# Optimization experiments

Hardware: AMD Instinct MI355X
Metric: run time of the kernel (lower is better)

The kernel has to match this reference:

```python
import jax, jax.numpy as jnp
import numpy as np

NTOKEN, NINP, NHID = 32000, 512, 1024
B, T = 64, 512


def setup_inputs() -> dict:
    key = jax.random.key(0)
    ks = jax.random.split(key, 12)
    inp = {}
    inp["input"] = jax.random.randint(ks[0], (B, T), 0, NTOKEN, dtype=jnp.int64)
    inp["hx"] = jnp.zeros((B, NHID), jnp.float32)
    inp["cx"] = jnp.zeros((B, NHID), jnp.float32)
    inp["seq_len"] = jax.random.randint(ks[1], (B,), 1, T + 1, dtype=jnp.int64)
    # parameters
    inp["emb_table"] = jax.random.uniform(ks[2], (NTOKEN, NINP), jnp.float32, -0.1, 0.1)
    s_ih = 1.0 / np.sqrt(NHID)
    inp["W_ih"] = jax.random.uniform(ks[3], (4 * NHID, NINP), jnp.float32, -s_ih, s_ih)
    inp["W_hh"] = jax.random.uniform(ks[4], (4 * NHID, NHID), jnp.float32, -s_ih, s_ih)
    inp["b_ih"] = jax.random.uniform(ks[5], (4 * NHID,), jnp.float32, -s_ih, s_ih)
    inp["b_hh"] = jax.random.uniform(ks[6], (4 * NHID,), jnp.float32, -s_ih, s_ih)
    h3 = NHID // 3
    s1 = 1.0 / np.sqrt(NHID)
    inp["fc1_W"] = jax.random.uniform(ks[7], (h3, NHID), jnp.float32, -s1, s1)
    inp["fc1_b"] = jax.random.uniform(ks[8], (h3,), jnp.float32, -s1, s1)
    s2 = 1.0 / np.sqrt(h3)
    inp["fc2_W"] = jax.random.uniform(ks[9], (2, h3), jnp.float32, -s2, s2)
    inp["fc2_b"] = jax.random.uniform(ks[10], (2,), jnp.float32, -s2, s2)
    return inp


def reference(input, hx, cx, seq_len, emb_table, W_ih, W_hh, b_ih, b_hh,
              fc1_W, fc1_b, fc2_W, fc2_b):
    # emb: [T, B, ninp] (input is [B, T], transposed as in torch)
    emb = emb_table[input.T]
    # precompute input projections for all timesteps: [T, B, 4H]
    x_proj = jnp.einsum('tbi,gi->tbg', emb, W_ih) + b_ih + b_hh

    def step(carry, xg):
        h, c = carry
        gates = xg + h @ W_hh.T  # [B, 4H]
        i, f, g, o = jnp.split(gates, 4, axis=-1)
        i = jax.nn.sigmoid(i)
        f = jax.nn.sigmoid(f)
        g = jnp.tanh(g)
        o = jax.nn.sigmoid(o)
        c = f * c + i * g
        h = o * jnp.tanh(c)
        return (h, c), h

    (hx, cx), outs = jax.lax.scan(step, (hx, cx), x_proj)  # outs: [T, B, H]

    # ragged mean pool over valid timesteps t < seq_len[b]
    t = outs.shape[0]
    mask = (jnp.arange(t)[:, None] < seq_len[None, :]).astype(outs.dtype)  # [T, B]
    feature = jnp.einsum('tbh,tb->bh', outs, mask) / seq_len[:, None].astype(outs.dtype)

    x = feature @ fc1_W.T + fc1_b
    x = x @ fc2_W.T + fc2_b
    logp = jax.nn.log_softmax(x, axis=-1)
    return logp, hx, cx
```

## Files before the change

### kernel.cpp

```cpp
#include <hip/hip_runtime.h>
#include <stdint.h>

#define NTOK  32000
#define NINP  512
#define NHID  1024
#define NBATCH 64
#define NTIME 512
#define NGATE 4096
#define H3    341

typedef __attribute__((ext_vector_type(8))) short  short8;
typedef __attribute__((ext_vector_type(4))) float  floatx4;
typedef unsigned long long ull;

#define HBUF_DW (NBATCH * NHID / 2)

__device__ __forceinline__ unsigned short f2bf(float f) {
  union { float f; unsigned u; } v; v.f = f;
  unsigned r = v.u + 0x7fffu + ((v.u >> 16) & 1u);
  return (unsigned short)(r >> 16);
}
__device__ __forceinline__ float bf2f(unsigned short h) {
  union { unsigned u; float f; } v; v.u = ((unsigned)h) << 16;
  return v.f;
}

__device__ __forceinline__ int pack2gate(int p) {
  int cb = p >> 7, r7 = p & 127;
  int w = r7 >> 5, r5 = r7 & 31;
  int uu = r5 >> 2, q = r5 & 3;
  int u = cb * 32 + w * 8 + uu;
  return q * NHID + u;
}


__global__ void k_pack_w(const float* __restrict__ src, unsigned short* __restrict__ dst, int K) {
  int p = blockIdx.x;
  int g = pack2gate(p);
  const float* s = src + (size_t)g * K;
  unsigned short* d = dst + (size_t)p * K;
  for (int k = threadIdx.x * 2; k < K; k += 512) {
    d[k] = f2bf(s[k]);
    d[k + 1] = f2bf(s[k + 1]);
  }
}

__global__ void k_bias(const float* __restrict__ bih, const float* __restrict__ bhh,
                       float* __restrict__ bp) {
  int p = blockIdx.x * 256 + threadIdx.x;
  if (p < NGATE) { int g = pack2gate(p); bp[p] = bih[g] + bhh[g]; }
}

__global__ void k_hbuf(const float* __restrict__ hx, unsigned short* __restrict__ hbuf) {
  int i = blockIdx.x * 256 + threadIdx.x;
  if (i < NBATCH * NHID) hbuf[i] = f2bf(hx[i]);
}

__global__ void k_gather(const int* __restrict__ input, const float* __restrict__ emb,
                         unsigned short* __restrict__ Ag, int t0, int Tc) {
  int total = Tc * 64 * (NINP / 8);
  for (int ci = blockIdx.x * 256 + threadIdx.x; ci < total; ci += gridDim.x * 256) {
    int row = ci >> 6;
    int k8 = (ci & 63) * 8;
    int b = row & 63;
    int tl = row >> 6;
    int tok = input[(size_t)b * NTIME + t0 + tl];
    const float* s = emb + (size_t)tok * NINP + k8;
    unsigned short* d = Ag + (size_t)row * NINP + k8;
#pragma unroll
    for (int j = 0; j < 8; ++j) d[j] = f2bf(s[j]);
  }
}


__global__ __launch_bounds__(256) void k_gemm(const unsigned short* __restrict__ Ag,
                                              const unsigned short* __restrict__ Wp,
                                              const float* __restrict__ biasP,
                                              unsigned short* __restrict__ xproj, int M) {
  __shared__ __attribute__((aligned(16))) unsigned short As[128 * 64];
  __shared__ __attribute__((aligned(16))) unsigned short Bs[128 * 64];
  const int tid = threadIdx.x;
  const int lane = tid & 63;
  const int w = tid >> 6;
  const int wr = w >> 1, wc = w & 1;
  const size_t rowbase = (size_t)blockIdx.x * 128;
  const int pbase = blockIdx.y * 128;

  floatx4 z = {0.f, 0.f, 0.f, 0.f};
  floatx4 acc[4][4];
#pragma unroll
  for (int i = 0; i < 4; ++i)
#pragma unroll
    for (int j = 0; j < 4; ++j) acc[i][j] = z;

  for (int kk = 0; kk < NINP; kk += 64) {
#pragma unroll
    for (int j = 0; j < 4; ++j) {
      int ci = j * 256 + tid;
      int r = ci >> 3;
      int kb = (ci & 7) * 16;
      int dst = r * 128 + (kb ^ ((r & 7) << 4));
      *(short8*)((char*)As + dst) =
          *(const short8*)((const char*)Ag + ((rowbase + r) * NINP + kk) * 2 + kb);
      *(short8*)((char*)Bs + dst) =
          *(const short8*)((const char*)Wp + ((size_t)(pbase + r) * NINP + kk) * 2 + kb);
    }
    __syncthreads();
#pragma unroll
    for (int k32 = 0; k32 < 2; ++k32) {
      short8 af[4], bfr[4];
      int kq = k32 * 64 + (lane >> 4) * 16;
#pragma unroll
      for (int t = 0; t < 4; ++t) {
        int r = wr * 64 + t * 16 + (lane & 15);
        af[t] = *(const short8*)((const char*)As + r * 128 + (kq ^ ((r & 7) << 4)));
        int cc = wc * 64 + t * 16 + (lane & 15);
        bfr[t] = *(const short8*)((const char*)Bs + cc * 128 + (kq ^ ((cc & 7) << 4)));
      }
#pragma unroll
      for (int tm = 0; tm < 4; ++tm)
#pragma unroll
        for (int tn = 0; tn < 4; ++tn)
          acc[tm][tn] = __builtin_amdgcn_mfma_f32_16x16x32_bf16(af[tm], bfr[tn], acc[tm][tn], 0, 0, 0);
    }
    __syncthreads();
  }
#pragma unroll
  for (int tn = 0; tn < 4; ++tn) {
    int p = pbase + wc * 64 + tn * 16 + (lane & 15);
    float bv = biasP[p];
#pragma unroll
    for (int tm = 0; tm < 4; ++tm) {
      size_t r0 = rowbase + wr * 64 + tm * 16 + ((lane >> 4) * 4);
#pragma unroll
      for (int j = 0; j < 4; ++j)
        xproj[(r0 + j) * NGATE + p] = f2bf(acc[tm][tn][j] + bv);
    }
  }
}


__global__ __launch_bounds__(256, 1) void k_rec(const unsigned short* __restrict__ Whp,
                                                const unsigned short* __restrict__ xproj,
                                                unsigned* __restrict__ hbuf,
                                                float* __restrict__ cbuf,
                                                float* __restrict__ featbuf,
                                                const float* __restrict__ cx_in,
                                                const int* __restrict__ seq_len,
                                                float* __restrict__ out,
                                                unsigned* __restrict__ flags, int t0, int Tc) {
  __shared__ __attribute__((aligned(16))) unsigned short hs[16 * NHID];
  __shared__ __attribute__((aligned(16))) unsigned short xs[8 * 128];
  __shared__ __attribute__((aligned(16))) float gs[4][32][8];

  const int tid = threadIdx.x;
  const int lane = tid & 63;
  const int w = tid >> 6;
  const int rg = blockIdx.x & 7;
  const int cb = blockIdx.x >> 3;
  const int colbase = cb * 128 + w * 32;

  {
    short8 zz = {0, 0, 0, 0, 0, 0, 0, 0};
    short8* zp = (short8*)(hs + 8 * NHID);
    for (int i = tid; i < 1024; i += 256) zp[i] = zz;
  }

  short8 wf[64];
  {
    const int c0 = lane & 15;
    const int ke = (lane >> 4) * 8;
#pragma unroll
    for (int i = 0; i < 64; ++i) {
      int kk = i >> 1, n = i & 1;
      wf[i] = *(const short8*)(Whp + (size_t)(colbase + n * 16 + c0) * NHID + kk * 32 + ke);
    }
  }

  const int urow = lane >> 3;
  const int uu = lane & 7;
  const int row_g = rg * 8 + urow;
  const int u_g = cb * 32 + w * 8 + uu;
  float c = (t0 == 0) ? cx_in[row_g * NHID + u_g] : cbuf[row_g * NHID + u_g];
  float feat = (t0 == 0) ? 0.f : featbuf[row_g * NHID + u_g];
  const int sl = seq_len[row_g];
  const bool self = ((lane & 31) == cb);

  short8 xreg;
  if (tid < 128) {
    int r = tid >> 4;
    int kb = (tid & 15) * 16;
    xreg = *(const short8*)((const char*)xproj +
                            ((size_t)(rg * 8 + r) * NGATE + cb * 128) * 2 + kb);
  }

  for (int tl = 0; tl < Tc; ++tl) {
    const int tglob = t0 + tl;
    const short8* hp =
        (const short8*)(hbuf + (size_t)(tglob & 1) * HBUF_DW + (size_t)rg * 8 * (NHID / 2));

    if (tid < 128) {
      int r = tid >> 4;
      int kb = (tid & 15) * 16;
      *(short8*)((char*)xs + r * 256 + kb) = xreg;
    }

    {
      short8 q0, q1, q2, q3;
      asm volatile(
          "global_load_dwordx4 %0, %4, off sc1\n\t"
          "global_load_dwordx4 %1, %5, off sc1\n\t"
          "global_load_dwordx4 %2, %6, off sc1\n\t"
          "global_load_dwordx4 %3, %7, off sc1\n\t"
          "s_waitcnt vmcnt(0)"
          : "=&v"(q0), "=&v"(q1), "=&v"(q2), "=&v"(q3)
          : "v"(hp + tid), "v"(hp + 256 + tid), "v"(hp + 512 + tid), "v"(hp + 768 + tid)
          : "memory");
      int ci, r, kb;
      ci = tid;       r = ci >> 7; kb = (ci & 127) * 16;
      *(short8*)((char*)hs + r * 2048 + (kb ^ ((r & 7) << 4))) = q0;
      ci = 256 + tid; r = ci >> 7; kb = (ci & 127) * 16;
      *(short8*)((char*)hs + r * 2048 + (kb ^ ((r & 7) << 4))) = q1;
      ci = 512 + tid; r = ci >> 7; kb = (ci & 127) * 16;
      *(short8*)((char*)hs + r * 2048 + (kb ^ ((r & 7) << 4))) = q2;
      ci = 768 + tid; r = ci >> 7; kb = (ci & 127) * 16;
      *(short8*)((char*)hs + r * 2048 + (kb ^ ((r & 7) << 4))) = q3;
    }
    __syncthreads();

    if (tid < 128 && tl + 1 < Tc) {
      int r = tid >> 4;
      int kb = (tid & 15) * 16;
      xreg = *(const short8*)((const char*)xproj +
                              ((size_t)((tl + 1) * 64 + rg * 8 + r) * NGATE + cb * 128) * 2 + kb);
    }

    floatx4 acc0a = {0.f, 0.f, 0.f, 0.f}, acc0b = {0.f, 0.f, 0.f, 0.f};
    floatx4 acc1a = {0.f, 0.f, 0.f, 0.f}, acc1b = {0.f, 0.f, 0.f, 0.f};
    {
      const int rr = lane & 15;
      const int kq = (lane >> 4) * 16;
#pragma unroll
      for (int kk = 0; kk < 32; kk += 2) {
        int kb0 = kk * 64 + kq;
        int kb1 = (kk + 1) * 64 + kq;
        short8 a0 = *(const short8*)((const char*)hs + rr * 2048 + (kb0 ^ ((rr & 7) << 4)));
        short8 a1 = *(const short8*)((const char*)hs + rr * 2048 + (kb1 ^ ((rr & 7) << 4)));
        acc0a = __builtin_amdgcn_mfma_f32_16x16x32_bf16(a0, wf[2 * kk + 0], acc0a, 0, 0, 0);
        acc1a = __builtin_amdgcn_mfma_f32_16x16x32_bf16(a0, wf[2 * kk + 1], acc1a, 0, 0, 0);
        acc0b = __builtin_amdgcn_mfma_f32_16x16x32_bf16(a1, wf[2 * kk + 2], acc0b, 0, 0, 0);
        acc1b = __builtin_amdgcn_mfma_f32_16x16x32_bf16(a1, wf[2 * kk + 3], acc1b, 0, 0, 0);
      }
    }
    floatx4 acc0 = acc0a + acc0b;
    floatx4 acc1 = acc1a + acc1b;

    if (lane < 32) {
      int r0 = (lane >> 4) * 4;
      int c0 = lane & 15;
      floatx4 g0, g1;
#pragma unroll
      for (int j = 0; j < 4; ++j) {
        g0[j] = acc0[j] + bf2f(xs[(r0 + j) * 128 + w * 32 + c0]);
        g1[j] = acc1[j] + bf2f(xs[(r0 + j) * 128 + w * 32 + c0 + 16]);
      }
      *(floatx4*)&gs[w][c0][r0] = g0;
      *(floatx4*)&gs[w][c0 + 16][r0] = g1;
    }

    float gi = gs[w][uu * 4 + 0][urow];
    float gf = gs[w][uu * 4 + 1][urow];
    float gg = gs[w][uu * 4 + 2][urow];
    float go = gs[w][uu * 4 + 3][urow];
    float si = 1.f / (1.f + __expf(-gi));
    float sf = 1.f / (1.f + __expf(-gf));
    float tg = tanhf(gg);
    float so = 1.f / (1.f + __expf(-go));
    c = sf * c + si * tg;
    float h = so * tanhf(c);
    if (tglob < sl) feat += h;

    {
      unsigned hb = (unsigned)f2bf(h);
      unsigned partner = (unsigned)__shfl_xor((int)hb, 1);
      if ((lane & 1) == 0) {
        unsigned packed = hb | (partner << 16);
        unsigned* dst = hbuf + (size_t)((tglob + 1) & 1) * HBUF_DW +
                        ((row_g * NHID + u_g) >> 1);
        __hip_atomic_store(dst, packed, __ATOMIC_RELAXED, __HIP_MEMORY_SCOPE_AGENT);
      }
    }
    if (tglob == NTIME - 1) out[128 + row_g * NHID + u_g] = h;

    asm volatile("s_waitcnt vmcnt(0)" ::: "memory");
    __syncthreads();
    unsigned target = (unsigned)(tglob + 1);
    if (tid == 0)
      __hip_atomic_store(flags + rg * 32 + cb, target, __ATOMIC_RELAXED,
                         __HIP_MEMORY_SCOPE_AGENT);
    {
      const unsigned* slot = flags + rg * 32 + (lane & 31);
      unsigned v = self ? 0xFFFFFFFFu
                        : __hip_atomic_load(slot, __ATOMIC_RELAXED, __HIP_MEMORY_SCOPE_AGENT);
      while (__any(v < target)) {
        v = self ? 0xFFFFFFFFu
                 : __hip_atomic_load(slot, __ATOMIC_RELAXED, __HIP_MEMORY_SCOPE_AGENT);
      }
    }
  }

  cbuf[row_g * NHID + u_g] = c;
  featbuf[row_g * NHID + u_g] = feat;
  if (t0 + Tc == NTIME) out[128 + NBATCH * NHID + row_g * NHID + u_g] = c;
}


__global__ void k_fc(const float* __restrict__ feat, const int* __restrict__ seq_len,
                     const float* __restrict__ w1, const float* __restrict__ b1,
                     const float* __restrict__ w2, const float* __restrict__ b2,
                     float* __restrict__ out) {
  int b = blockIdx.x;
  int tid = threadIdx.x;
  __shared__ float fs[NHID];
  __shared__ float x1s[H3 + 3];
  float inv = 1.f / (float)seq_len[b];
  for (int i = tid; i < NHID; i += 256) fs[i] = feat[(size_t)b * NHID + i] * inv;
  __syncthreads();
  for (int j = tid; j < H3; j += 256) {
    const float* wr = w1 + (size_t)j * NHID;
    float s = b1[j];
    for (int k = 0; k < NHID; k += 4)
      s += fs[k] * wr[k] + fs[k + 1] * wr[k + 1] + fs[k + 2] * wr[k + 2] + fs[k + 3] * wr[k + 3];
    x1s[j] = s;
  }
  __syncthreads();
  if (tid == 0) {
    float l0 = b2[0], l1 = b2[1];
    for (int k = 0; k < H3; ++k) {
      l0 += w2[k] * x1s[k];
      l1 += w2[H3 + k] * x1s[k];
    }
    float m = fmaxf(l0, l1);
    float lse = m + logf(__expf(l0 - m) + __expf(l1 - m));
    out[b * 2 + 0] = l0 - lse;
    out[b * 2 + 1] = l1 - lse;
  }
}


extern "C" void kernel_launch(void* const* d_in, const int* in_sizes, int n_in, void* d_out,
                              int out_size, void* d_ws, size_t ws_size, hipStream_t stream) {
  const int* input = (const int*)d_in[0];
  const float* hx = (const float*)d_in[1];
  const float* cx = (const float*)d_in[2];
  const int* seq_len = (const int*)d_in[3];
  const float* emb = (const float*)d_in[4];
  const float* W_ih = (const float*)d_in[5];
  const float* W_hh = (const float*)d_in[6];
  const float* b_ih = (const float*)d_in[7];
  const float* b_hh = (const float*)d_in[8];
  const float* fc1W = (const float*)d_in[9];
  const float* fc1b = (const float*)d_in[10];
  const float* fc2W = (const float*)d_in[11];
  const float* fc2b = (const float*)d_in[12];
  float* out = (float*)d_out;

  char* ws = (char*)d_ws;
  size_t off = 0;
  auto take = [&](size_t n) {
    char* p = ws + off;
    off = (off + n + 255) & ~(size_t)255;
    return p;
  };
  unsigned short* WihP = (unsigned short*)take((size_t)NGATE * NINP * 2);
  unsigned short* WhhP = (unsigned short*)take((size_t)NGATE * NHID * 2);
  float* biasP = (float*)take(NGATE * 4);
  unsigned* hbuf = (unsigned*)take((size_t)2 * HBUF_DW * 4);
  float* cbuf = (float*)take((size_t)NBATCH * NHID * 4);
  float* featbuf = (float*)take((size_t)NBATCH * NHID * 4);
  unsigned* flags = (unsigned*)take(8 * 32 * 4);
  size_t fixed = off;

  int Tc = 512;
  while (Tc > 8) {
    size_t need = fixed + ((size_t)Tc * 64 * NINP * 2 + 256) + ((size_t)Tc * 64 * NGATE * 2 + 256);
    if (need <= ws_size) break;
    Tc >>= 1;
  }
  unsigned short* Ag = (unsigned short*)take((size_t)Tc * 64 * NINP * 2);
  unsigned short* xproj = (unsigned short*)take((size_t)Tc * 64 * NGATE * 2);

  k_pack_w<<<NGATE, 256, 0, stream>>>(W_ih, WihP, NINP);
  k_pack_w<<<NGATE, 256, 0, stream>>>(W_hh, WhhP, NHID);
  k_bias<<<NGATE / 256, 256, 0, stream>>>(b_ih, b_hh, biasP);
  k_hbuf<<<NBATCH * NHID / 256, 256, 0, stream>>>(hx, (unsigned short*)hbuf);
  hipMemsetAsync(flags, 0, 8 * 32 * 4, stream);

  for (int t0 = 0; t0 < NTIME; t0 += Tc) {
    k_gather<<<256, 256, 0, stream>>>(input, emb, Ag, t0, Tc);
    k_gemm<<<dim3(Tc * 64 / 128, NGATE / 128), 256, 0, stream>>>(Ag, WihP, biasP, xproj, Tc * 64);
    k_rec<<<256, 256, 0, stream>>>(WhhP, xproj, hbuf, cbuf, featbuf, cx, seq_len, out, flags, t0, Tc);
  }
  k_fc<<<NBATCH, 256, 0, stream>>>(featbuf, seq_len, fc1W, fc1b, fc2W, fc2b, out);
}
```

Baseline: 2.082 ms.

## Use per-wave flags, double-buffered h smem, and MFMA-fragment xproj layout

Rewrites the GEMM epilogue so xproj is stored in the exact per-lane MFMA fragment order. Each wave of the recurrent kernel then loads its input-projection slice straight into registers, with no shared staging buffer. The recurrent step double-buffers the h tile in shared memory and swaps the block-wide barrier plus per-block flag for per-wave flags, so waves signal and poll independently. It also software-pipelines the LDS loads of h ahead of the MFMAs and reads only 8 real rows instead of padding to 16. These changes shorten the per-timestep critical path, at the cost of polling more flags (256 per row group instead of 32) and scattered 2-byte global stores in the GEMM epilogue.

```diff
diff --git a/kernel.cpp b/kernel.cpp
--- a/kernel.cpp
+++ b/kernel.cpp
@@ -76,7 +76,7 @@
 __global__ __launch_bounds__(256) void k_gemm(const unsigned short* __restrict__ Ag,
                                               const unsigned short* __restrict__ Wp,
                                               const float* __restrict__ biasP,
-                                              unsigned short* __restrict__ xproj, int M) {
+                                              unsigned short* __restrict__ xprojF, int M) {
   __shared__ __attribute__((aligned(16))) unsigned short As[128 * 64];
   __shared__ __attribute__((aligned(16))) unsigned short Bs[128 * 64];
   const int tid = threadIdx.x;
@@ -129,19 +129,28 @@
   for (int tn = 0; tn < 4; ++tn) {
     int p = pbase + wc * 64 + tn * 16 + (lane & 15);
     float bv = biasP[p];
+    int cb2 = p >> 7, w2 = (p >> 5) & 3, c5 = p & 31;
+    int s = c5 >> 4, c0b = c5 & 15;
 #pragma unroll
     for (int tm = 0; tm < 4; ++tm) {
       size_t r0 = rowbase + wr * 64 + tm * 16 + ((lane >> 4) * 4);
 #pragma unroll
-      for (int j = 0; j < 4; ++j)
-        xproj[(r0 + j) * NGATE + p] = f2bf(acc[tm][tn][j] + bv);
+      for (int j = 0; j < 4; ++j) {
+        size_t r = r0 + j;
+        int tl2 = (int)(r >> 6), b = (int)(r & 63);
+        int rg2 = b >> 3, ur = b & 7;
+        int l2 = ((ur >> 2) << 4) | c0b;
+        size_t idx = ((((size_t)(tl2 * 8 + rg2) * 32 + cb2) * 4 + w2) * 32 + l2) * 8 +
+                     (size_t)(ur & 3) * 2 + s;
+        xprojF[idx] = f2bf(acc[tm][tn][j] + bv);
+      }
     }
   }
 }
 
 
 __global__ __launch_bounds__(256, 1) void k_rec(const unsigned short* __restrict__ Whp,
-                                                const unsigned short* __restrict__ xproj,
+                                                const unsigned short* __restrict__ xprojF,
                                                 unsigned* __restrict__ hbuf,
                                                 float* __restrict__ cbuf,
                                                 float* __restrict__ featbuf,
@@ -149,8 +158,7 @@
                                                 const int* __restrict__ seq_len,
                                                 float* __restrict__ out,
                                                 unsigned* __restrict__ flags, int t0, int Tc) {
-  __shared__ __attribute__((aligned(16))) unsigned short hs[16 * NHID];
-  __shared__ __attribute__((aligned(16))) unsigned short xs[8 * 128];
+  __shared__ __attribute__((aligned(16))) unsigned short hs[2][8 * NHID];
   __shared__ __attribute__((aligned(16))) float gs[4][32][8];
 
   const int tid = threadIdx.x;
@@ -159,12 +167,6 @@
   const int rg = blockIdx.x & 7;
   const int cb = blockIdx.x >> 3;
   const int colbase = cb * 128 + w * 32;
-
-  {
-    short8 zz = {0, 0, 0, 0, 0, 0, 0, 0};
-    short8* zp = (short8*)(hs + 8 * NHID);
-    for (int i = tid; i < 1024; i += 256) zp[i] = zz;
-  }
 
   short8 wf[64];
   {
@@ -184,26 +186,18 @@
   float c = (t0 == 0) ? cx_in[row_g * NHID + u_g] : cbuf[row_g * NHID + u_g];
   float feat = (t0 == 0) ? 0.f : featbuf[row_g * NHID + u_g];
   const int sl = seq_len[row_g];
-  const bool self = ((lane & 31) == cb);
-
-  short8 xreg;
-  if (tid < 128) {
-    int r = tid >> 4;
-    int kb = (tid & 15) * 16;
-    xreg = *(const short8*)((const char*)xproj +
-                            ((size_t)(rg * 8 + r) * NGATE + cb * 128) * 2 + kb);
-  }
+
+  const char* xB = (const char*)xprojF;
+  short8 xr = {0, 0, 0, 0, 0, 0, 0, 0};
+  if (lane < 32)
+    xr = *(const short8*)(xB + ((((size_t)0 * 8 + rg) * 32 + cb) * 4 + w) * 512 + (size_t)lane * 16);
 
   for (int tl = 0; tl < Tc; ++tl) {
     const int tglob = t0 + tl;
+    const int buf = tglob & 1;
     const short8* hp =
-        (const short8*)(hbuf + (size_t)(tglob & 1) * HBUF_DW + (size_t)rg * 8 * (NHID / 2));
-
-    if (tid < 128) {
-      int r = tid >> 4;
-      int kb = (tid & 15) * 16;
-      *(short8*)((char*)xs + r * 256 + kb) = xreg;
-    }
+        (const short8*)(hbuf + (size_t)buf * HBUF_DW + (size_t)rg * 8 * (NHID / 2));
+    unsigned short* hsb = hs[buf];
 
     {
       short8 q0, q1, q2, q3;
@@ -218,38 +212,42 @@
           : "memory");
       int ci, r, kb;
       ci = tid;       r = ci >> 7; kb = (ci & 127) * 16;
-      *(short8*)((char*)hs + r * 2048 + (kb ^ ((r & 7) << 4))) = q0;
+      *(short8*)((char*)hsb + r * 2048 + (kb ^ ((r & 7) << 4))) = q0;
       ci = 256 + tid; r = ci >> 7; kb = (ci & 127) * 16;
-      *(short8*)((char*)hs + r * 2048 + (kb ^ ((r & 7) << 4))) = q1;
+      *(short8*)((char*)hsb + r * 2048 + (kb ^ ((r & 7) << 4))) = q1;
       ci = 512 + tid; r = ci >> 7; kb = (ci & 127) * 16;
-      *(short8*)((char*)hs + r * 2048 + (kb ^ ((r & 7) << 4))) = q2;
+      *(short8*)((char*)hsb + r * 2048 + (kb ^ ((r & 7) << 4))) = q2;
       ci = 768 + tid; r = ci >> 7; kb = (ci & 127) * 16;
-      *(short8*)((char*)hs + r * 2048 + (kb ^ ((r & 7) << 4))) = q3;
+      *(short8*)((char*)hsb + r * 2048 + (kb ^ ((r & 7) << 4))) = q3;
     }
     __syncthreads();
 
-    if (tid < 128 && tl + 1 < Tc) {
-      int r = tid >> 4;
-      int kb = (tid & 15) * 16;
-      xreg = *(const short8*)((const char*)xproj +
-                              ((size_t)((tl + 1) * 64 + rg * 8 + r) * NGATE + cb * 128) * 2 + kb);
-    }
+    short8 xr2 = {0, 0, 0, 0, 0, 0, 0, 0};
+    if (lane < 32 && tl + 1 < Tc)
+      xr2 = *(const short8*)(xB + ((((size_t)(tl + 1) * 8 + rg) * 32 + cb) * 4 + w) * 512 +
+                             (size_t)lane * 16);
 
     floatx4 acc0a = {0.f, 0.f, 0.f, 0.f}, acc0b = {0.f, 0.f, 0.f, 0.f};
     floatx4 acc1a = {0.f, 0.f, 0.f, 0.f}, acc1b = {0.f, 0.f, 0.f, 0.f};
     {
-      const int rr = lane & 15;
+      const int rrc = lane & 7;
       const int kq = (lane >> 4) * 16;
+      const char* hrow = (const char*)hsb + rrc * 2048;
+      const int sw = rrc << 4;
+      short8 aA = *(const short8*)(hrow + ((0 * 64 + kq) ^ sw));
+      short8 aB = *(const short8*)(hrow + ((1 * 64 + kq) ^ sw));
 #pragma unroll
       for (int kk = 0; kk < 32; kk += 2) {
-        int kb0 = kk * 64 + kq;
-        int kb1 = (kk + 1) * 64 + kq;
-        short8 a0 = *(const short8*)((const char*)hs + rr * 2048 + (kb0 ^ ((rr & 7) << 4)));
-        short8 a1 = *(const short8*)((const char*)hs + rr * 2048 + (kb1 ^ ((rr & 7) << 4)));
-        acc0a = __builtin_amdgcn_mfma_f32_16x16x32_bf16(a0, wf[2 * kk + 0], acc0a, 0, 0, 0);
-        acc1a = __builtin_amdgcn_mfma_f32_16x16x32_bf16(a0, wf[2 * kk + 1], acc1a, 0, 0, 0);
-        acc0b = __builtin_amdgcn_mfma_f32_16x16x32_bf16(a1, wf[2 * kk + 2], acc0b, 0, 0, 0);
-        acc1b = __builtin_amdgcn_mfma_f32_16x16x32_bf16(a1, wf[2 * kk + 3], acc1b, 0, 0, 0);
+        short8 nA = aA, nB = aB;
+        if (kk < 30) {
+          nA = *(const short8*)(hrow + (((kk + 2) * 64 + kq) ^ sw));
+          nB = *(const short8*)(hrow + (((kk + 3) * 64 + kq) ^ sw));
+        }
+        acc0a = __builtin_amdgcn_mfma_f32_16x16x32_bf16(aA, wf[2 * kk + 0], acc0a, 0, 0, 0);
+        acc1a = __builtin_amdgcn_mfma_f32_16x16x32_bf16(aA, wf[2 * kk + 1], acc1a, 0, 0, 0);
+        acc0b = __builtin_amdgcn_mfma_f32_16x16x32_bf16(aB, wf[2 * kk + 2], acc0b, 0, 0, 0);
+        acc1b = __builtin_amdgcn_mfma_f32_16x16x32_bf16(aB, wf[2 * kk + 3], acc1b, 0, 0, 0);
+        aA = nA; aB = nB;
       }
     }
     floatx4 acc0 = acc0a + acc0b;
@@ -261,12 +259,13 @@
       floatx4 g0, g1;
 #pragma unroll
       for (int j = 0; j < 4; ++j) {
-        g0[j] = acc0[j] + bf2f(xs[(r0 + j) * 128 + w * 32 + c0]);
-        g1[j] = acc1[j] + bf2f(xs[(r0 + j) * 128 + w * 32 + c0 + 16]);
+        g0[j] = acc0[j] + bf2f((unsigned short)xr[j * 2 + 0]);
+        g1[j] = acc1[j] + bf2f((unsigned short)xr[j * 2 + 1]);
       }
       *(floatx4*)&gs[w][c0][r0] = g0;
       *(floatx4*)&gs[w][c0 + 16][r0] = g1;
     }
+    xr = xr2;
 
     float gi = gs[w][uu * 4 + 0][urow];
     float gf = gs[w][uu * 4 + 1][urow];
@@ -293,18 +292,17 @@
     if (tglob == NTIME - 1) out[128 + row_g * NHID + u_g] = h;
 
     asm volatile("s_waitcnt vmcnt(0)" ::: "memory");
-    __syncthreads();
     unsigned target = (unsigned)(tglob + 1);
-    if (tid == 0)
-      __hip_atomic_store(flags + rg * 32 + cb, target, __ATOMIC_RELAXED,
+    if (lane == 0)
+      __hip_atomic_store(flags + rg * 128 + cb * 4 + w, target, __ATOMIC_RELAXED,
                          __HIP_MEMORY_SCOPE_AGENT);
     {
-      const unsigned* slot = flags + rg * 32 + (lane & 31);
-      unsigned v = self ? 0xFFFFFFFFu
-                        : __hip_atomic_load(slot, __ATOMIC_RELAXED, __HIP_MEMORY_SCOPE_AGENT);
-      while (__any(v < target)) {
-        v = self ? 0xFFFFFFFFu
-                 : __hip_atomic_load(slot, __ATOMIC_RELAXED, __HIP_MEMORY_SCOPE_AGENT);
+      const unsigned* fb = flags + rg * 128;
+      unsigned v0 = __hip_atomic_load(fb + lane, __ATOMIC_RELAXED, __HIP_MEMORY_SCOPE_AGENT);
+      unsigned v1 = __hip_atomic_load(fb + 64 + lane, __ATOMIC_RELAXED, __HIP_MEMORY_SCOPE_AGENT);
+      while (__any((v0 < target) || (v1 < target))) {
+        v0 = __hip_atomic_load(fb + lane, __ATOMIC_RELAXED, __HIP_MEMORY_SCOPE_AGENT);
+        v1 = __hip_atomic_load(fb + 64 + lane, __ATOMIC_RELAXED, __HIP_MEMORY_SCOPE_AGENT);
       }
     }
   }
@@ -378,7 +376,7 @@
   unsigned* hbuf = (unsigned*)take((size_t)2 * HBUF_DW * 4);
   float* cbuf = (float*)take((size_t)NBATCH * NHID * 4);
   float* featbuf = (float*)take((size_t)NBATCH * NHID * 4);
-  unsigned* flags = (unsigned*)take(8 * 32 * 4);
+  unsigned* flags = (unsigned*)take(8 * 128 * 4);
   size_t fixed = off;
 
   int Tc = 512;
@@ -388,18 +386,18 @@
     Tc >>= 1;
   }
   unsigned short* Ag = (unsigned short*)take((size_t)Tc * 64 * NINP * 2);
-  unsigned short* xproj = (unsigned short*)take((size_t)Tc * 64 * NGATE * 2);
+  unsigned short* xprojF = (unsigned short*)take((size_t)Tc * 64 * NGATE * 2);
 
   k_pack_w<<<NGATE, 256, 0, stream>>>(W_ih, WihP, NINP);
   k_pack_w<<<NGATE, 256, 0, stream>>>(W_hh, WhhP, NHID);
   k_bias<<<NGATE / 256, 256, 0, stream>>>(b_ih, b_hh, biasP);
   k_hbuf<<<NBATCH * NHID / 256, 256, 0, stream>>>(hx, (unsigned short*)hbuf);
-  hipMemsetAsync(flags, 0, 8 * 32 * 4, stream);
+  hipMemsetAsync(flags, 0, 8 * 128 * 4, stream);
 
   for (int t0 = 0; t0 < NTIME; t0 += Tc) {
     k_gather<<<256, 256, 0, stream>>>(input, emb, Ag, t0, Tc);
-    k_gemm<<<dim3(Tc * 64 / 128, NGATE / 128), 256, 0, stream>>>(Ag, WihP, biasP, xproj, Tc * 64);
-    k_rec<<<256, 256, 0, stream>>>(WhhP, xproj, hbuf, cbuf, featbuf, cx, seq_len, out, flags, t0, Tc);
+    k_gemm<<<dim3(Tc * 64 / 128, NGATE / 128), 256, 0, stream>>>(Ag, WihP, biasP, xprojF, Tc * 64);
+    k_rec<<<256, 256, 0, stream>>>(WhhP, xprojF, hbuf, cbuf, featbuf, cx, seq_len, out, flags, t0, Tc);
   }
   k_fc<<<NBATCH, 256, 0, stream>>>(featbuf, seq_len, fc1W, fc1b, fc2W, fc2b, out);
 }
```

New measurement: 5.872 ms. +182.1%, slower.

## Split h-state load into two K halves overlapping load with MFMA

Applied to the files above, without the earlier changes.

The per-timestep hidden-state fetch from global memory is split into two halves along K. The first half is staged to LDS and its MFMAs start while the second half's loads are still in flight. The second half is waited on, stored, and then computed. The aim is to hide part of the global load latency on the serial recurrence critical path, at the cost of one extra __syncthreads per step.

```diff
diff --git a/kernel.cpp b/kernel.cpp
--- a/kernel.cpp
+++ b/kernel.cpp
@@ -205,29 +205,6 @@
       *(short8*)((char*)xs + r * 256 + kb) = xreg;
     }
 
-    {
-      short8 q0, q1, q2, q3;
-      asm volatile(
-          "global_load_dwordx4 %0, %4, off sc1\n\t"
-          "global_load_dwordx4 %1, %5, off sc1\n\t"
-          "global_load_dwordx4 %2, %6, off sc1\n\t"
-          "global_load_dwordx4 %3, %7, off sc1\n\t"
-          "s_waitcnt vmcnt(0)"
-          : "=&v"(q0), "=&v"(q1), "=&v"(q2), "=&v"(q3)
-          : "v"(hp + tid), "v"(hp + 256 + tid), "v"(hp + 512 + tid), "v"(hp + 768 + tid)
-          : "memory");
-      int ci, r, kb;
-      ci = tid;       r = ci >> 7; kb = (ci & 127) * 16;
-      *(short8*)((char*)hs + r * 2048 + (kb ^ ((r & 7) << 4))) = q0;
-      ci = 256 + tid; r = ci >> 7; kb = (ci & 127) * 16;
-      *(short8*)((char*)hs + r * 2048 + (kb ^ ((r & 7) << 4))) = q1;
-      ci = 512 + tid; r = ci >> 7; kb = (ci & 127) * 16;
-      *(short8*)((char*)hs + r * 2048 + (kb ^ ((r & 7) << 4))) = q2;
-      ci = 768 + tid; r = ci >> 7; kb = (ci & 127) * 16;
-      *(short8*)((char*)hs + r * 2048 + (kb ^ ((r & 7) << 4))) = q3;
-    }
-    __syncthreads();
-
     if (tid < 128 && tl + 1 < Tc) {
       int r = tid >> 4;
       int kb = (tid & 15) * 16;
@@ -235,22 +212,62 @@
                               ((size_t)((tl + 1) * 64 + rg * 8 + r) * NGATE + cb * 128) * 2 + kb);
     }
 
+    const int r01 = tid >> 6;
+    const int r45 = 4 + r01;
+    const int cw = tid & 63;
+    const short8* a0p = hp + r01 * 128 + cw;
+    const short8* a1p = hp + r45 * 128 + cw;
+    short8 q0, q1, q2, q3;
+    asm volatile(
+        "global_load_dwordx4 %0, %4, off sc1\n\t"
+        "global_load_dwordx4 %1, %5, off sc1\n\t"
+        "global_load_dwordx4 %2, %6, off sc1\n\t"
+        "global_load_dwordx4 %3, %7, off sc1\n\t"
+        "s_waitcnt vmcnt(2)"
+        : "=&v"(q0), "=&v"(q1), "=&v"(q2), "=&v"(q3)
+        : "v"(a0p), "v"(a1p), "v"(a0p + 64), "v"(a1p + 64)
+        : "memory");
+    {
+      int kb = cw * 16;
+      *(short8*)((char*)hs + r01 * 2048 + (kb ^ ((r01 & 7) << 4))) = q0;
+      *(short8*)((char*)hs + r45 * 2048 + (kb ^ ((r45 & 7) << 4))) = q1;
+    }
+    __syncthreads();
+
     floatx4 acc0a = {0.f, 0.f, 0.f, 0.f}, acc0b = {0.f, 0.f, 0.f, 0.f};
     floatx4 acc1a = {0.f, 0.f, 0.f, 0.f}, acc1b = {0.f, 0.f, 0.f, 0.f};
+    const int rr = lane & 15;
+    const int kq = (lane >> 4) * 16;
+#pragma unroll
+    for (int kk = 0; kk < 16; kk += 2) {
+      int kb0 = kk * 64 + kq;
+      int kb1 = (kk + 1) * 64 + kq;
+      short8 a0 = *(const short8*)((const char*)hs + rr * 2048 + (kb0 ^ ((rr & 7) << 4)));
+      short8 a1 = *(const short8*)((const char*)hs + rr * 2048 + (kb1 ^ ((rr & 7) << 4)));
+      acc0a = __builtin_amdgcn_mfma_f32_16x16x32_bf16(a0, wf[2 * kk + 0], acc0a, 0, 0, 0);
+      acc1a = __builtin_amdgcn_mfma_f32_16x16x32_bf16(a0, wf[2 * kk + 1], acc1a, 0, 0, 0);
+      acc0b = __builtin_amdgcn_mfma_f32_16x16x32_bf16(a1, wf[2 * kk + 2], acc0b, 0, 0, 0);
+      acc1b = __builtin_amdgcn_mfma_f32_16x16x32_bf16(a1, wf[2 * kk + 3], acc1b, 0, 0, 0);
+    }
+
+    asm volatile("s_waitcnt vmcnt(0)" : "+v"(q2), "+v"(q3) :: "memory");
     {
-      const int rr = lane & 15;
-      const int kq = (lane >> 4) * 16;
-#pragma unroll
-      for (int kk = 0; kk < 32; kk += 2) {
-        int kb0 = kk * 64 + kq;
-        int kb1 = (kk + 1) * 64 + kq;
-        short8 a0 = *(const short8*)((const char*)hs + rr * 2048 + (kb0 ^ ((rr & 7) << 4)));
-        short8 a1 = *(const short8*)((const char*)hs + rr * 2048 + (kb1 ^ ((rr & 7) << 4)));
-        acc0a = __builtin_amdgcn_mfma_f32_16x16x32_bf16(a0, wf[2 * kk + 0], acc0a, 0, 0, 0);
-        acc1a = __builtin_amdgcn_mfma_f32_16x16x32_bf16(a0, wf[2 * kk + 1], acc1a, 0, 0, 0);
-        acc0b = __builtin_amdgcn_mfma_f32_16x16x32_bf16(a1, wf[2 * kk + 2], acc0b, 0, 0, 0);
-        acc1b = __builtin_amdgcn_mfma_f32_16x16x32_bf16(a1, wf[2 * kk + 3], acc1b, 0, 0, 0);
-      }
+      int kb = 1024 + cw * 16;
+      *(short8*)((char*)hs + r01 * 2048 + (kb ^ ((r01 & 7) << 4))) = q2;
+      *(short8*)((char*)hs + r45 * 2048 + (kb ^ ((r45 & 7) << 4))) = q3;
+    }
+    __syncthreads();
+
+#pragma unroll
+    for (int kk = 16; kk < 32; kk += 2) {
+      int kb0 = kk * 64 + kq;
+      int kb1 = (kk + 1) * 64 + kq;
+      short8 a0 = *(const short8*)((const char*)hs + rr * 2048 + (kb0 ^ ((rr & 7) << 4)));
+      short8 a1 = *(const short8*)((const char*)hs + rr * 2048 + (kb1 ^ ((rr & 7) << 4)));
+      acc0a = __builtin_amdgcn_mfma_f32_16x16x32_bf16(a0, wf[2 * kk + 0], acc0a, 0, 0, 0);
+      acc1a = __builtin_amdgcn_mfma_f32_16x16x32_bf16(a0, wf[2 * kk + 1], acc1a, 0, 0, 0);
+      acc0b = __builtin_amdgcn_mfma_f32_16x16x32_bf16(a1, wf[2 * kk + 2], acc0b, 0, 0, 0);
+      acc1b = __builtin_amdgcn_mfma_f32_16x16x32_bf16(a1, wf[2 * kk + 3], acc1b, 0, 0, 0);
     }
     floatx4 acc0 = acc0a + acc0b;
     floatx4 acc1 = acc1a + acc1b;
```

New measurement: 1.957 ms. 1.06x faster.
